# Kernel tuning notes

Hardware: AMD Instinct MI355X
Metric: run time of the kernel (lower is better)

The kernel has to match this reference:

```python
import jax, jax.numpy as jnp
import numpy as np

H = 2048      # hidden_size
I = 8192      # intermediate_size
NH = 16       # num_heads
HD = H // NH  # head_dim
EPS = 1e-6


def setup_inputs() -> dict:
    key = jax.random.key(0)
    ks = jax.random.split(key, 10)
    s = 0.02
    return {
        "hidden_states": jax.random.normal(ks[0], (2, 2048, H), dtype=jnp.float32),
        "wq": jax.random.normal(ks[1], (H, H), dtype=jnp.float32) * s,
        "wk": jax.random.normal(ks[2], (H, H), dtype=jnp.float32) * s,
        "wv": jax.random.normal(ks[3], (H, H), dtype=jnp.float32) * s,
        "wo": jax.random.normal(ks[4], (H, H), dtype=jnp.float32) * s,
        "w_gate": jax.random.normal(ks[5], (H, I), dtype=jnp.float32) * s,
        "w_up": jax.random.normal(ks[6], (H, I), dtype=jnp.float32) * s,
        "w_down": jax.random.normal(ks[7], (I, H), dtype=jnp.float32) * s,
        "ln1_w": jnp.ones((H,), dtype=jnp.float32),
        "ln2_w": jnp.ones((H,), dtype=jnp.float32),
    }


def rmsnorm(x, w):
    xf = x.astype(jnp.float32)
    var = jnp.mean(xf * xf, axis=-1, keepdims=True)
    return w * (xf * jax.lax.rsqrt(var + EPS)).astype(x.dtype)


def reference(hidden_states, wq, wk, wv, wo, w_gate, w_up, w_down, ln1_w, ln2_w):
    b, s, _ = hidden_states.shape
    residual = hidden_states
    x = rmsnorm(hidden_states, ln1_w)

    # attention (no RoPE, no causal mask, per source)
    q = (x @ wq).reshape(b, s, NH, HD)
    k = (x @ wk).reshape(b, s, NH, HD)
    v = (x @ wv).reshape(b, s, NH, HD)
    scores = jnp.einsum('bqhd,bkhd->bhqk', q, k) / jnp.sqrt(jnp.float32(HD))
    attn = jax.nn.softmax(scores, axis=-1)
    out = jnp.einsum('bhqk,bkhd->bqhd', attn, v).reshape(b, s, H)
    hidden = residual + out @ wo

    residual = hidden
    y = rmsnorm(hidden, ln2_w)
    gate = jax.nn.silu(y @ w_gate)
    up = y @ w_up
    return residual + (gate * up) @ w_down
```

## Files before the change

### kernel.cpp

```cpp
#include <hip/hip_runtime.h>
#include <hip/hip_bf16.h>

#define HDIM 2048
#define IDIM 8192
#define NHEADS 16
#define HEADD 128
#define BATCH 2
#define SEQ 2048
#define MTOK 4096

typedef unsigned short u16;
typedef __bf16 bf16x8 __attribute__((ext_vector_type(8)));
typedef float f32x4 __attribute__((ext_vector_type(4)));
typedef float f32x16 __attribute__((ext_vector_type(16)));
typedef unsigned short u16x8 __attribute__((ext_vector_type(8)));
typedef unsigned int u32x2 __attribute__((ext_vector_type(2)));
typedef unsigned int u32x4 __attribute__((ext_vector_type(4)));
typedef unsigned int uv2 __attribute__((ext_vector_type(2)));

__device__ __forceinline__ u16 f2b(float f) {
  unsigned u = __builtin_bit_cast(unsigned, f);
  u += 0x7FFFu + ((u >> 16) & 1u);
  return (u16)(u >> 16);
}
__device__ __forceinline__ float b2f(u16 b) {
  unsigned u = ((unsigned)b) << 16;
  return __builtin_bit_cast(float, u);
}
__device__ __forceinline__ void gl_lds16(const void* g, void* l) {
  auto gp = (const __attribute__((address_space(1))) unsigned int*)((unsigned long long)g);
  auto lp = (__attribute__((address_space(3))) unsigned int*)((unsigned)(unsigned long long)l);
  __builtin_amdgcn_global_load_lds(gp, lp, 16, 0, 0);
}
__device__ __forceinline__ unsigned cvtpk(float lo, float hi) {
  unsigned r;
  asm("v_cvt_pk_bf16_f32 %0, %1, %2" : "=v"(r) : "v"(lo), "v"(hi));
  return r;
}

__global__ __launch_bounds__(256) void wtrans_k(const float* __restrict__ W, u16* __restrict__ Wt,
                                                int K, int N, int rowoff) {
  __shared__ float t[64][65];
  int n0 = blockIdx.x * 64, k0 = blockIdx.y * 64;
  int tid = threadIdx.x;
  int kr = tid >> 4, nc = (tid & 15) * 4;
#pragma unroll
  for (int p = 0; p < 4; p++) {
    float4 v = *(const float4*)&W[(size_t)(k0 + p * 16 + kr) * N + n0 + nc];
    t[nc + 0][p * 16 + kr] = v.x;
    t[nc + 1][p * 16 + kr] = v.y;
    t[nc + 2][p * 16 + kr] = v.z;
    t[nc + 3][p * 16 + kr] = v.w;
  }
  __syncthreads();
  int n = tid >> 2, kq = (tid & 3) * 16;
  u16 tmp[16];
#pragma unroll
  for (int i = 0; i < 16; i++) tmp[i] = f2b(t[n][kq + i]);
  *(u16x8*)&Wt[(size_t)(rowoff + n0 + n) * K + k0 + kq] = *(u16x8*)&tmp[0];
  *(u16x8*)&Wt[(size_t)(rowoff + n0 + n) * K + k0 + kq + 8] = *(u16x8*)&tmp[8];
}

__global__ __launch_bounds__(256) void vtrans_k(const u16* __restrict__ qkv, u16* __restrict__ vt) {
  __shared__ u16 t[32][33];
  int s0 = blockIdx.x * 32, d0 = blockIdx.y * 32, bh = blockIdx.z;
  int b = bh >> 4, h = bh & 15;
  int tx = threadIdx.x, ty = threadIdx.y;
#pragma unroll
  for (int i = 0; i < 4; i++)
    t[ty + i * 8][tx] = qkv[(size_t)(b * SEQ + s0 + ty + i * 8) * 6144 + 4096 + h * HEADD + d0 + tx];
  __syncthreads();
#pragma unroll
  for (int i = 0; i < 4; i++)
    vt[(size_t)(bh * HEADD + d0 + ty + i * 8) * SEQ + s0 + tx] = t[tx][ty + i * 8];
}

__global__ __launch_bounds__(256) void rmsnorm_k(const float* __restrict__ X, const float* __restrict__ W,
                                                 u16* __restrict__ O) {
  int row = blockIdx.x;
  int tid = threadIdx.x;
  const float* x = X + (size_t)row * HDIM;
  float4 v0 = ((const float4*)x)[tid * 2];
  float4 v1 = ((const float4*)x)[tid * 2 + 1];
  float ss = v0.x * v0.x + v0.y * v0.y + v0.z * v0.z + v0.w * v0.w
           + v1.x * v1.x + v1.y * v1.y + v1.z * v1.z + v1.w * v1.w;
#pragma unroll
  for (int off = 32; off > 0; off >>= 1) ss += __shfl_down(ss, off);
  __shared__ float red[4];
  if ((tid & 63) == 0) red[tid >> 6] = ss;
  __syncthreads();
  float rs = rsqrtf((red[0] + red[1] + red[2] + red[3]) * (1.0f / HDIM) + 1e-6f);
  const float* w = W + tid * 8;
  u16* o = O + (size_t)row * HDIM + tid * 8;
  float vals[8] = {v0.x, v0.y, v0.z, v0.w, v1.x, v1.y, v1.z, v1.w};
#pragma unroll
  for (int j = 0; j < 8; j++) o[j] = f2b(w[j] * vals[j] * rs);
}

template <int EPI>
__global__ __launch_bounds__(512, 2) void gemm256(const u16* __restrict__ A, const u16* __restrict__ Bt,
                                                  int M, int N, int K,
                                                  u16* __restrict__ Cb, float* __restrict__ Cf,
                                                  const float* __restrict__ Res, u16* __restrict__ Gm) {
  __shared__ char lds[98304];
  const int tid = threadIdx.x;
  const int lane = tid & 63, w = tid >> 6;
  const int wm = w >> 1, wn = w & 1;
  const int nwg = gridDim.x * gridDim.y;
  const int bid = blockIdx.y * gridDim.x + blockIdx.x;
  const int swz = (bid & 7) * (nwg >> 3) + (bid >> 3);
  const int bx = swz % gridDim.x, by = swz / gridDim.x;
  const int n0 = bx * 128, m0 = by * 256;
  const int NT = K >> 6;

  const int r8 = lane >> 3, s8 = lane & 7;
  const int slog8 = (s8 ^ r8) * 8;
  const u16* Abase = A + (size_t)(m0 + w * 8 + r8) * K + slog8;
  const u16* Bbase = Bt + (size_t)(n0 + w * 8 + r8) * K + slog8;
  const int stA = w * 1024;

#define STAGE_A(buf, kt, h)                                                        \
  {                                                                                \
    const u16* s_ = Abase + (size_t)(h) * 128 * K + (size_t)(kt) * 64;             \
    gl_lds16(s_, lds + (buf) * 49152 + (h) * 16384 + stA);                         \
    gl_lds16(s_ + 64 * (size_t)K, lds + (buf) * 49152 + (h) * 16384 + stA + 8192); \
  }
#define STAGE_B(buf, kt)                                                     \
  {                                                                          \
    const u16* s_ = Bbase + (size_t)(kt) * 64;                               \
    gl_lds16(s_, lds + (buf) * 49152 + 32768 + stA);                         \
    gl_lds16(s_ + 64 * (size_t)K, lds + (buf) * 49152 + 32768 + stA + 8192); \
  }
#define LG0 { asm volatile("s_waitcnt lgkmcnt(0)" ::: "memory"); __builtin_amdgcn_sched_barrier(0); }

  const int l15 = lane & 15, l4 = lane >> 4;
  const int kq0 = (l4 * 16) ^ ((lane & 7) << 4);
  const int kq1 = (64 + l4 * 16) ^ ((lane & 7) << 4);
  const int aro = (wm >> 1) * 16384 + ((wm & 1) * 64 + l15) * 128;
  const int bro = 32768 + (wn * 64 + l15) * 128;

  const f32x4 fz = {0.f, 0.f, 0.f, 0.f};
  f32x4 acc[4][4];
#pragma unroll
  for (int i = 0; i < 4; i++)
#pragma unroll
    for (int j = 0; j < 4; j++) acc[i][j] = fz;
  bf16x8 af[4][2], bfr[4][2];

  STAGE_A(0, 0, 0);
  STAGE_A(0, 0, 1);
  STAGE_B(0, 0);
  STAGE_A(1, 1, 0);
  STAGE_A(1, 1, 1);
  asm volatile("s_waitcnt vmcnt(4)" ::: "memory");
  __builtin_amdgcn_s_barrier();

  for (int t = 0; t < NT; ++t) {
    const int buf = t & 1;
    const char* Lb = lds + buf * 49152;
    const int t1 = (t + 1 < NT) ? t + 1 : NT - 1;
    const int t2 = (t + 2 < NT) ? t + 2 : NT - 1;
    if (wm < 2) {
#pragma unroll
      for (int mf = 0; mf < 4; mf++) {
        af[mf][0] = *(const bf16x8*)(Lb + aro + mf * 2048 + kq0);
        af[mf][1] = *(const bf16x8*)(Lb + aro + mf * 2048 + kq1);
      }
    } else {
#pragma unroll
      for (int mf = 0; mf < 4; mf++)
        af[mf][0] = *(const bf16x8*)(Lb + aro + mf * 2048 + kq0);
    }
#pragma unroll
    for (int nf = 0; nf < 4; nf++)
      bfr[nf][0] = *(const bf16x8*)(Lb + bro + nf * 2048 + kq0);
    STAGE_B((t + 1) & 1, t1);
    __builtin_amdgcn_s_barrier();
    LG0;
    __builtin_amdgcn_s_setprio(1);
#pragma unroll
    for (int nf = 0; nf < 4; nf++) {
      acc[0][nf] = __builtin_amdgcn_mfma_f32_16x16x32_bf16(af[0][0], bfr[nf][0], acc[0][nf], 0, 0, 0);
      acc[1][nf] = __builtin_amdgcn_mfma_f32_16x16x32_bf16(af[1][0], bfr[nf][0], acc[1][nf], 0, 0, 0);
    }
    __builtin_amdgcn_s_setprio(0);
    __builtin_amdgcn_s_barrier();
    if (wm >= 2) {
#pragma unroll
      for (int mf = 0; mf < 4; mf++)
        af[mf][1] = *(const bf16x8*)(Lb + aro + mf * 2048 + kq1);
    }
#pragma unroll
    for (int nf = 0; nf < 4; nf++)
      bfr[nf][1] = *(const bf16x8*)(Lb + bro + nf * 2048 + kq1);
    STAGE_A(buf, t2, 0);
    __builtin_amdgcn_s_barrier();
    LG0;
    __builtin_amdgcn_s_setprio(1);
#pragma unroll
    for (int nf = 0; nf < 4; nf++) {
      acc[2][nf] = __builtin_amdgcn_mfma_f32_16x16x32_bf16(af[2][0], bfr[nf][0], acc[2][nf], 0, 0, 0);
      acc[3][nf] = __builtin_amdgcn_mfma_f32_16x16x32_bf16(af[3][0], bfr[nf][0], acc[3][nf], 0, 0, 0);
    }
    __builtin_amdgcn_s_setprio(0);
    __builtin_amdgcn_s_barrier();
    STAGE_A(buf, t2, 1);
    __builtin_amdgcn_s_barrier();
    LG0;
    __builtin_amdgcn_s_setprio(1);
#pragma unroll
    for (int nf = 0; nf < 4; nf++) {
      acc[0][nf] = __builtin_amdgcn_mfma_f32_16x16x32_bf16(af[0][1], bfr[nf][1], acc[0][nf], 0, 0, 0);
      acc[1][nf] = __builtin_amdgcn_mfma_f32_16x16x32_bf16(af[1][1], bfr[nf][1], acc[1][nf], 0, 0, 0);
    }
    __builtin_amdgcn_s_setprio(0);
    __builtin_amdgcn_s_barrier();
    __builtin_amdgcn_s_setprio(1);
#pragma unroll
    for (int nf = 0; nf < 4; nf++) {
      acc[2][nf] = __builtin_amdgcn_mfma_f32_16x16x32_bf16(af[2][1], bfr[nf][1], acc[2][nf], 0, 0, 0);
      acc[3][nf] = __builtin_amdgcn_mfma_f32_16x16x32_bf16(af[3][1], bfr[nf][1], acc[3][nf], 0, 0, 0);
    }
    __builtin_amdgcn_s_setprio(0);
    asm volatile("s_waitcnt vmcnt(4)" ::: "memory");
    __builtin_amdgcn_s_barrier();
  }
  asm volatile("s_waitcnt vmcnt(0)" ::: "memory");

  const int r0 = l4 * 4;
#pragma unroll
  for (int mf = 0; mf < 4; mf++) {
#pragma unroll
    for (int j = 0; j < 4; j++) {
      const int m = m0 + wm * 64 + mf * 16 + r0 + j;
#pragma unroll
      for (int nf = 0; nf < 4; nf++) {
        const int n = n0 + wn * 64 + nf * 16 + l15;
        float v = acc[mf][nf][j];
        size_t idx = (size_t)m * N + n;
        if (EPI == 0) {
          Cb[idx] = f2b(v);
        } else if (EPI == 1) {
          float sg = v / (1.f + __expf(-v));
          Cb[idx] = f2b(sg);
        } else if (EPI == 2) {
          float gv = b2f(Gm[idx]);
          Gm[idx] = f2b(gv * v);
        } else {
          Cf[idx] = Res[idx] + v;
        }
      }
    }
  }
#undef STAGE_A
#undef STAGE_B
#undef LG0
}

__global__ __launch_bounds__(512, 2) void attn_k(const u16* __restrict__ qkv, const u16* __restrict__ vt,
                                                 u16* __restrict__ out) {
  __shared__ char Kl[2][16384];
  __shared__ char Vl[2][16384];
  int tid = threadIdx.x, lane = tid & 63, w = tid >> 6;
  int bid = blockIdx.y * 8 + blockIdx.x;
  int swz = (bid & 7) * 32 + (bid >> 3);
  int qb = swz & 7, bh = swz >> 3;
  int b = bh >> 4, h = bh & 15;
  int l31 = lane & 31, hi = lane >> 5;
  const float c = 0.088388347648318447f * 1.4426950408889634f;
  const float RT = 90.51f;

  const int qrow = qb * 256 + w * 32 + l31;
  bf16x8 q[8];
  {
    const u16* qp = qkv + (size_t)(b * SEQ + qrow) * 6144 + h * HEADD + hi * 8;
#pragma unroll
    for (int dt = 0; dt < 8; dt++) q[dt] = *(const bf16x8*)(qp + dt * 16);
  }
  f32x16 o[4];
#pragma unroll
  for (int i = 0; i < 4; i++)
#pragma unroll
    for (int j = 0; j < 16; j++) o[i][j] = 0.f;
  float mrow = -1e30f, lrow = 0.f;

#define ASTAGE(buf, t)                                                                     \
  {                                                                                        \
    int kv0_ = (t) * 64;                                                                   \
    _Pragma("unroll") for (int i = 0; i < 2; i++) {                                        \
      int r = w * 8 + i * 4 + (lane >> 4);                                                 \
      int col = ((lane & 15) ^ (r & 15)) * 8;                                              \
      const u16* src = qkv + (size_t)(b * SEQ + kv0_ + r) * 6144 + HDIM + h * HEADD + col; \
      gl_lds16(src, &Kl[buf][(w * 8 + i * 4) * 256]);                                      \
    }                                                                                      \
    _Pragma("unroll") for (int i = 0; i < 2; i++) {                                        \
      int d = w * 16 + i * 8 + (lane >> 3);                                                \
      int col = ((lane & 7) ^ (d & 7)) * 8;                                                \
      const u16* src = vt + (size_t)(bh * HEADD + d) * SEQ + kv0_ + col;                   \
      gl_lds16(src, &Vl[buf][(w * 16 + i * 8) * 128]);                                     \
    }                                                                                      \
  }

  ASTAGE(0, 0);
  __syncthreads();

  for (int t = 0; t < SEQ / 64; t++) {
    const int buf = t & 1;
    if (t + 1 < SEQ / 64) ASTAGE(buf ^ 1, t + 1);
    const char* Kb = &Kl[buf][0];
    const char* Vb = &Vl[buf][0];
    f32x16 s0, s1;
#pragma unroll
    for (int j = 0; j < 16; j++) { s0[j] = 0.f; s1[j] = 0.f; }
    const int ksl = l31 & 15;
    __builtin_amdgcn_s_setprio(1);
#pragma unroll
    for (int dt = 0; dt < 8; dt++) {
      bf16x8 k0 = *(const bf16x8*)(Kb + (l31)*256 + (((dt * 2 + hi) ^ ksl) << 4));
      bf16x8 k1 = *(const bf16x8*)(Kb + (32 + l31) * 256 + (((dt * 2 + hi) ^ ksl) << 4));
      s0 = __builtin_amdgcn_mfma_f32_32x32x16_bf16(k0, q[dt], s0, 0, 0, 0);
      s1 = __builtin_amdgcn_mfma_f32_32x32x16_bf16(k1, q[dt], s1, 0, 0, 0);
    }
    __builtin_amdgcn_s_setprio(0);
    float m8[8];
#pragma unroll
    for (int g = 0; g < 4; g++) {
      m8[g] = fmaxf(fmaxf(s0[4 * g], s0[4 * g + 1]), fmaxf(s0[4 * g + 2], s0[4 * g + 3]));
      m8[4 + g] = fmaxf(fmaxf(s1[4 * g], s1[4 * g + 1]), fmaxf(s1[4 * g + 2], s1[4 * g + 3]));
    }
    float vmax = fmaxf(fmaxf(fmaxf(m8[0], m8[1]), fmaxf(m8[2], m8[3])),
                       fmaxf(fmaxf(m8[4], m8[5]), fmaxf(m8[6], m8[7])));
    {
      uv2 pr = __builtin_amdgcn_permlane32_swap(__builtin_bit_cast(unsigned, vmax),
                                                __builtin_bit_cast(unsigned, vmax), false, false);
      vmax = fmaxf(__builtin_bit_cast(float, pr[0]), __builtin_bit_cast(float, pr[1]));
    }
    if (__any(vmax > mrow + RT)) {
      float mnew = fmaxf(mrow, vmax);
      float alpha = exp2f((mrow - mnew) * c);
      mrow = mnew;
      lrow *= alpha;
#pragma unroll
      for (int i = 0; i < 4; i++)
#pragma unroll
        for (int j = 0; j < 16; j++) o[i][j] *= alpha;
    }
    const float mc = mrow * c;
    float r4[4] = {0.f, 0.f, 0.f, 0.f};
#pragma unroll
    for (int j = 0; j < 16; j++) {
      s0[j] = exp2f(s0[j] * c - mc);
      r4[j & 3] += s0[j];
    }
#pragma unroll
    for (int j = 0; j < 16; j++) {
      s1[j] = exp2f(s1[j] * c - mc);
      r4[j & 3] += s1[j];
    }
    float rsum = (r4[0] + r4[1]) + (r4[2] + r4[3]);
    {
      uv2 pr = __builtin_amdgcn_permlane32_swap(__builtin_bit_cast(unsigned, rsum),
                                                __builtin_bit_cast(unsigned, rsum), false, false);
      rsum = __builtin_bit_cast(float, pr[0]) + __builtin_bit_cast(float, pr[1]);
    }
    lrow += rsum;
    bf16x8 pa[4];
#pragma unroll
    for (int half = 0; half < 2; half++) {
      const f32x16& sv = half ? s1 : s0;
#pragma unroll
      for (int blk = 0; blk < 2; blk++) {
        int base = blk * 8;
        unsigned A = cvtpk(sv[base + 0], sv[base + 1]);
        unsigned B = cvtpk(sv[base + 2], sv[base + 3]);
        unsigned C = cvtpk(sv[base + 4], sv[base + 5]);
        unsigned D = cvtpk(sv[base + 6], sv[base + 7]);
        uv2 ac = __builtin_amdgcn_permlane32_swap(A, C, false, false);
        uv2 bd = __builtin_amdgcn_permlane32_swap(B, D, false, false);
        u32x4 w4;
        w4[0] = ac[0]; w4[1] = bd[0]; w4[2] = ac[1]; w4[3] = bd[1];
        pa[half * 2 + blk] = __builtin_bit_cast(bf16x8, w4);
      }
    }
    __builtin_amdgcn_s_setprio(1);
#pragma unroll
    for (int dt4 = 0; dt4 < 4; dt4++) {
      const char* vbase = Vb + (dt4 * 32 + l31) * 128;
      const int vsl = l31 & 7;
#pragma unroll
      for (int ks = 0; ks < 4; ks++) {
        bf16x8 vb = *(const bf16x8*)(vbase + (((ks * 2 + hi) ^ vsl) << 4));
        o[dt4] = __builtin_amdgcn_mfma_f32_32x32x16_bf16(vb, pa[ks], o[dt4], 0, 0, 0);
      }
    }
    __builtin_amdgcn_s_setprio(0);
    __syncthreads();
  }
#undef ASTAGE

  const float linv = 1.0f / lrow;
  u16* orow = out + (size_t)(b * SEQ + qrow) * HDIM + h * HEADD;
#pragma unroll
  for (int dt4 = 0; dt4 < 4; dt4++) {
#pragma unroll
    for (int g = 0; g < 4; g++) {
      u32x2 st;
      st[0] = cvtpk(o[dt4][4 * g + 0] * linv, o[dt4][4 * g + 1] * linv);
      st[1] = cvtpk(o[dt4][4 * g + 2] * linv, o[dt4][4 * g + 3] * linv);
      *(u32x2*)(orow + dt4 * 32 + 8 * g + 4 * hi) = st;
    }
  }
}

extern "C" void kernel_launch(void* const* d_in, const int* in_sizes, int n_in,
                              void* d_out, int out_size, void* d_ws, size_t ws_size,
                              hipStream_t stream) {
  const float* hs  = (const float*)d_in[0];
  const float* wq  = (const float*)d_in[1];
  const float* wk  = (const float*)d_in[2];
  const float* wv  = (const float*)d_in[3];
  const float* wo  = (const float*)d_in[4];
  const float* wg  = (const float*)d_in[5];
  const float* wu  = (const float*)d_in[6];
  const float* wd  = (const float*)d_in[7];
  const float* ln1 = (const float*)d_in[8];
  const float* ln2 = (const float*)d_in[9];
  char* ws = (char*)d_ws;
  u16*   wqkvT = (u16*)(ws);
  u16*   woT   = (u16*)(ws + 25165824ull);
  u16*   wgT   = (u16*)(ws + 33554432ull);
  u16*   wuT   = (u16*)(ws + 67108864ull);
  u16*   wdT   = (u16*)(ws + 100663296ull);
  u16*   xb    = (u16*)(ws + 134217728ull);
  float* hid   = (float*)(ws + 150994944ull);
  u16*   qkv   = (u16*)(ws + 184549376ull);
  u16*   vtb   = (u16*)(ws + 234881024ull);
  u16*   attn  = (u16*)(ws + 251658368ull);
  u16*   g     = qkv;

  wtrans_k<<<dim3(32, 32), 256, 0, stream>>>(wq, wqkvT, HDIM, HDIM, 0);
  wtrans_k<<<dim3(32, 32), 256, 0, stream>>>(wk, wqkvT, HDIM, HDIM, 2048);
  wtrans_k<<<dim3(32, 32), 256, 0, stream>>>(wv, wqkvT, HDIM, HDIM, 4096);
  wtrans_k<<<dim3(32, 32), 256, 0, stream>>>(wo, woT, HDIM, HDIM, 0);
  wtrans_k<<<dim3(128, 32), 256, 0, stream>>>(wg, wgT, HDIM, IDIM, 0);
  wtrans_k<<<dim3(128, 32), 256, 0, stream>>>(wu, wuT, HDIM, IDIM, 0);
  wtrans_k<<<dim3(32, 128), 256, 0, stream>>>(wd, wdT, IDIM, HDIM, 0);

  rmsnorm_k<<<MTOK, 256, 0, stream>>>(hs, ln1, xb);
  gemm256<0><<<dim3(48, 16), 512, 0, stream>>>(xb, wqkvT, MTOK, 6144, HDIM, qkv, nullptr, nullptr, nullptr);
  vtrans_k<<<dim3(64, 4, 32), dim3(32, 8), 0, stream>>>(qkv, vtb);
  attn_k<<<dim3(8, 32), 512, 0, stream>>>(qkv, vtb, attn);
  gemm256<3><<<dim3(16, 16), 512, 0, stream>>>(attn, woT, MTOK, HDIM, HDIM, nullptr, hid, hs, nullptr);
  rmsnorm_k<<<MTOK, 256, 0, stream>>>(hid, ln2, xb);
  gemm256<1><<<dim3(64, 16), 512, 0, stream>>>(xb, wgT, MTOK, IDIM, HDIM, g, nullptr, nullptr, nullptr);
  gemm256<2><<<dim3(64, 16), 512, 0, stream>>>(xb, wuT, MTOK, IDIM, HDIM, nullptr, nullptr, nullptr, g);
  gemm256<3><<<dim3(16, 16), 512, 0, stream>>>(g, wdT, MTOK, HDIM, IDIM, nullptr, (float*)d_out, hid, nullptr);
}
```

Before: 808.0 us.

## Add 256x256-tile GEMM with XCD-grouped scheduling for QKV and gate/up projections

Adds a new GEMM kernel that uses 256x256 output tiles with a 2x4 wave layout and 128KB of LDS. It double-buffers the A and B halves, interleaves global-to-LDS staging between MFMA phases, and raises wave priority around the MFMA bursts. Block IDs are remapped so each XCD works on a 4x4 group of neighbouring tiles, which should improve L2 reuse. The aim is higher arithmetic intensity per LDS byte and fewer redundant global loads for the large projection GEMMs. In exchange, register pressure rises and the grid has fewer workgroups, which could hurt occupancy or load balance.

Result: faster. 773.4 us (-4.3%).

```diff
diff --git a/kernel.cpp b/kernel.cpp
--- a/kernel.cpp
+++ b/kernel.cpp
@@ -95,6 +95,165 @@
   float vals[8] = {v0.x, v0.y, v0.z, v0.w, v1.x, v1.y, v1.z, v1.w};
 #pragma unroll
   for (int j = 0; j < 8; j++) o[j] = f2b(w[j] * vals[j] * rs);
+}
+
+template <int EPI>
+__global__ __launch_bounds__(512, 2) void gemm_w(const u16* __restrict__ A, const u16* __restrict__ Bt,
+                                                 int M, int N, int K,
+                                                 u16* __restrict__ Cb, float* __restrict__ Cf,
+                                                 const float* __restrict__ Res, u16* __restrict__ Gm) {
+  __shared__ char lds[131072];
+  const int tid = threadIdx.x;
+  const int lane = tid & 63, w = tid >> 6;
+  const int wm = w >> 2, wn = w & 3;
+  const int bid = blockIdx.y * gridDim.x + blockIdx.x;
+  const int xcd = bid & 7, idx = bid >> 3;
+  const int round = idx >> 4, j = idx & 15;
+  const int nsy4 = gridDim.y >> 2;
+  const int st = round * 8 + xcd;
+  const int sx = st / nsy4, syi = st % nsy4;
+  const int by = syi * 4 + (j & 3), bx = sx * 4 + (j >> 2);
+  const int m0 = by * 256, n0 = bx * 256;
+  const int NT = K >> 6;
+
+  const int srow = w * 8 + (lane >> 3);
+  const int kko = ((lane & 7) ^ (lane >> 3)) * 8;
+  const u16* Asrc = A + (size_t)(m0 + srow) * K + kko;
+  const u16* Bsrc = Bt + (size_t)(n0 + srow) * K + kko;
+  const int wofs = w * 1024;
+
+#define STAGE_AH(buf, kt, h)                                                          \
+  {                                                                                   \
+    gl_lds16(Asrc + ((size_t)((h) * 128) * K) + (size_t)(kt) * 64,                    \
+             lds + (buf) * 65536 + (h) * 16384 + wofs);                               \
+    gl_lds16(Asrc + ((size_t)((h) * 128 + 64) * K) + (size_t)(kt) * 64,               \
+             lds + (buf) * 65536 + (h) * 16384 + 8192 + wofs);                        \
+  }
+#define STAGE_BH(buf, kt, h)                                                          \
+  {                                                                                   \
+    gl_lds16(Bsrc + ((size_t)((h) * 128) * K) + (size_t)(kt) * 64,                    \
+             lds + (buf) * 65536 + 32768 + (h) * 16384 + wofs);                       \
+    gl_lds16(Bsrc + ((size_t)((h) * 128 + 64) * K) + (size_t)(kt) * 64,               \
+             lds + (buf) * 65536 + 32768 + (h) * 16384 + 8192 + wofs);                \
+  }
+#define LG0 { asm volatile("s_waitcnt lgkmcnt(0)" ::: "memory"); __builtin_amdgcn_sched_barrier(0); }
+
+  const int l15 = lane & 15, l4 = lane >> 4;
+  const int kq0 = ((l4) ^ (l15 & 7)) << 4;
+  const int kq1 = ((4 + l4) ^ (l15 & 7)) << 4;
+  const int abase = wm * 16384 + l15 * 128;
+  const int bbase = 32768 + (wn >> 1) * 16384 + ((wn & 1) * 64 + l15) * 128;
+
+  const f32x4 fz = {0.f, 0.f, 0.f, 0.f};
+  f32x4 acc[8][4];
+#pragma unroll
+  for (int i = 0; i < 8; i++)
+#pragma unroll
+    for (int jj = 0; jj < 4; jj++) acc[i][jj] = fz;
+  bf16x8 af[4], bfr[4];
+
+  STAGE_AH(0, 0, 0);
+  STAGE_AH(0, 0, 1);
+  STAGE_BH(0, 0, 0);
+  STAGE_BH(0, 0, 1);
+  STAGE_AH(1, 1, 0);
+  STAGE_BH(1, 1, 0);
+  asm volatile("s_waitcnt vmcnt(4)" ::: "memory");
+  __builtin_amdgcn_s_barrier();
+
+  for (int t = 0; t < NT; ++t) {
+    const int buf = t & 1, nbuf = buf ^ 1;
+    const char* Lb = lds + buf * 65536;
+    const int t1 = (t + 1 < NT) ? t + 1 : NT - 1;
+    const int t2 = (t + 2 < NT) ? t + 2 : NT - 1;
+#pragma unroll
+    for (int mf = 0; mf < 4; mf++) af[mf] = *(const bf16x8*)(Lb + abase + mf * 2048 + kq0);
+#pragma unroll
+    for (int nf = 0; nf < 4; nf++) bfr[nf] = *(const bf16x8*)(Lb + bbase + nf * 2048 + kq0);
+    STAGE_AH(nbuf, t1, 1);
+    STAGE_BH(nbuf, t1, 1);
+    __builtin_amdgcn_s_barrier();
+    LG0;
+    __builtin_amdgcn_s_setprio(1);
+#pragma unroll
+    for (int mf = 0; mf < 4; mf++)
+#pragma unroll
+      for (int nf = 0; nf < 4; nf++)
+        acc[mf][nf] = __builtin_amdgcn_mfma_f32_16x16x32_bf16(af[mf], bfr[nf], acc[mf][nf], 0, 0, 0);
+    __builtin_amdgcn_s_setprio(0);
+    __builtin_amdgcn_s_barrier();
+#pragma unroll
+    for (int mf = 0; mf < 4; mf++) af[mf] = *(const bf16x8*)(Lb + abase + (mf + 4) * 2048 + kq0);
+    __builtin_amdgcn_s_barrier();
+    LG0;
+    __builtin_amdgcn_s_setprio(1);
+#pragma unroll
+    for (int mf = 0; mf < 4; mf++)
+#pragma unroll
+      for (int nf = 0; nf < 4; nf++)
+        acc[mf + 4][nf] = __builtin_amdgcn_mfma_f32_16x16x32_bf16(af[mf], bfr[nf], acc[mf + 4][nf], 0, 0, 0);
+    __builtin_amdgcn_s_setprio(0);
+    __builtin_amdgcn_s_barrier();
+#pragma unroll
+    for (int mf = 0; mf < 4; mf++) af[mf] = *(const bf16x8*)(Lb + abase + mf * 2048 + kq1);
+#pragma unroll
+    for (int nf = 0; nf < 4; nf++) bfr[nf] = *(const bf16x8*)(Lb + bbase + nf * 2048 + kq1);
+    __builtin_amdgcn_s_barrier();
+    LG0;
+    __builtin_amdgcn_s_setprio(1);
+#pragma unroll
+    for (int mf = 0; mf < 4; mf++)
+#pragma unroll
+      for (int nf = 0; nf < 4; nf++)
+        acc[mf][nf] = __builtin_amdgcn_mfma_f32_16x16x32_bf16(af[mf], bfr[nf], acc[mf][nf], 0, 0, 0);
+    __builtin_amdgcn_s_setprio(0);
+    __builtin_amdgcn_s_barrier();
+#pragma unroll
+    for (int mf = 0; mf < 4; mf++) af[mf] = *(const bf16x8*)(Lb + abase + (mf + 4) * 2048 + kq1);
+    STAGE_AH(buf, t2, 0);
+    STAGE_BH(buf, t2, 0);
+    __builtin_amdgcn_s_barrier();
+    LG0;
+    __builtin_amdgcn_s_setprio(1);
+#pragma unroll
+    for (int mf = 0; mf < 4; mf++)
+#pragma unroll
+      for (int nf = 0; nf < 4; nf++)
+        acc[mf + 4][nf] = __builtin_amdgcn_mfma_f32_16x16x32_bf16(af[mf], bfr[nf], acc[mf + 4][nf], 0, 0, 0);
+    __builtin_amdgcn_s_setprio(0);
+    asm volatile("s_waitcnt vmcnt(4)" ::: "memory");
+    __builtin_amdgcn_s_barrier();
+  }
+  asm volatile("s_waitcnt vmcnt(0)" ::: "memory");
+
+  const int r0 = l4 * 4;
+#pragma unroll
+  for (int mf = 0; mf < 8; mf++) {
+#pragma unroll
+    for (int jr = 0; jr < 4; jr++) {
+      const int m = m0 + wm * 128 + mf * 16 + r0 + jr;
+#pragma unroll
+      for (int nf = 0; nf < 4; nf++) {
+        const int n = n0 + wn * 64 + nf * 16 + l15;
+        float v = acc[mf][nf][jr];
+        size_t idx = (size_t)m * N + n;
+        if (EPI == 0) {
+          Cb[idx] = f2b(v);
+        } else if (EPI == 1) {
+          float sg = v / (1.f + __expf(-v));
+          Cb[idx] = f2b(sg);
+        } else if (EPI == 2) {
+          float gv = b2f(Gm[idx]);
+          Gm[idx] = f2b(gv * v);
+        } else {
+          Cf[idx] = Res[idx] + v;
+        }
+      }
+    }
+  }
+#undef STAGE_AH
+#undef STAGE_BH
+#undef LG0
 }
 
 template <int EPI>
@@ -447,12 +606,12 @@
   wtrans_k<<<dim3(32, 128), 256, 0, stream>>>(wd, wdT, IDIM, HDIM, 0);
 
   rmsnorm_k<<<MTOK, 256, 0, stream>>>(hs, ln1, xb);
-  gemm256<0><<<dim3(48, 16), 512, 0, stream>>>(xb, wqkvT, MTOK, 6144, HDIM, qkv, nullptr, nullptr, nullptr);
+  gemm_w<0><<<dim3(24, 16), 512, 0, stream>>>(xb, wqkvT, MTOK, 6144, HDIM, qkv, nullptr, nullptr, nullptr);
   vtrans_k<<<dim3(64, 4, 32), dim3(32, 8), 0, stream>>>(qkv, vtb);
   attn_k<<<dim3(8, 32), 512, 0, stream>>>(qkv, vtb, attn);
   gemm256<3><<<dim3(16, 16), 512, 0, stream>>>(attn, woT, MTOK, HDIM, HDIM, nullptr, hid, hs, nullptr);
   rmsnorm_k<<<MTOK, 256, 0, stream>>>(hid, ln2, xb);
-  gemm256<1><<<dim3(64, 16), 512, 0, stream>>>(xb, wgT, MTOK, IDIM, HDIM, g, nullptr, nullptr, nullptr);
-  gemm256<2><<<dim3(64, 16), 512, 0, stream>>>(xb, wuT, MTOK, IDIM, HDIM, nullptr, nullptr, nullptr, g);
+  gemm_w<1><<<dim3(32, 16), 512, 0, stream>>>(xb, wgT, MTOK, IDIM, HDIM, g, nullptr, nullptr, nullptr);
+  gemm_w<2><<<dim3(32, 16), 512, 0, stream>>>(xb, wuT, MTOK, IDIM, HDIM, nullptr, nullptr, nullptr, g);
   gemm256<3><<<dim3(16, 16), 512, 0, stream>>>(g, wdT, MTOK, HDIM, IDIM, nullptr, (float*)d_out, hid, nullptr);
 }
```
